# Kernel optimization log

Hardware: AMD Instinct MI355X
Metric: run time of the kernel (lower is better)

Reference implementation:

```python
import jax, jax.numpy as jnp
import numpy as np

B, H, I = 64, 4096, 14336   # batch, hidden, expert intermediate
NLUT = 4096                 # 2**L_bits, L=12
W_SCALE = 0.02              # payload['W_scale'] (same for all three here)


def _rademacher(key, shape):
    return jnp.where(jax.random.bernoulli(key, 0.5, shape), 1.0, -1.0).astype(jnp.float32)


def setup_inputs() -> dict:
    key = jax.random.key(0)
    ks = jax.random.split(key, 14)
    inp = {
        "x": jax.random.normal(ks[0], (B, H), jnp.float32),
        "lut_gate": jax.random.normal(ks[1], (NLUT,), jnp.float32) * 0.05,
        "lut_up": jax.random.normal(ks[2], (NLUT,), jnp.float32) * 0.05,
        "lut_down": jax.random.normal(ks[3], (NLUT,), jnp.float32) * 0.05,
        "gate_walks": jax.random.randint(ks[4], (I, H), 0, NLUT, jnp.int32),
        "up_walks": jax.random.randint(ks[5], (I, H), 0, NLUT, jnp.int32),
        "down_walks": jax.random.randint(ks[6], (H, I), 0, NLUT, jnp.int32),
        "gate_sign_l": _rademacher(ks[7], (I,)),
        "gate_sign_r": _rademacher(ks[8], (H,)),
        "up_sign_l": _rademacher(ks[9], (I,)),
        "up_sign_r": _rademacher(ks[10], (H,)),
        "down_sign_l": _rademacher(ks[11], (H,)),
        "down_sign_r": _rademacher(ks[12], (I,)),
    }
    return inp


def _dequant(lut, walks, sign_l, sign_r):
    # trellis-walk LUT gather per weight element, then row/col signs and scalar scale
    # walks: (out, in) int codes; lut: (NLUT,)
    return (lut[walks] * sign_l[:, None] * sign_r[None, :]) * W_SCALE


def reference(x, lut_gate, lut_up, lut_down,
              gate_walks, up_walks, down_walks,
              gate_sign_l, gate_sign_r, up_sign_l, up_sign_r,
              down_sign_l, down_sign_r):
    W_gate = _dequant(lut_gate, gate_walks, gate_sign_l, gate_sign_r)  # (I, H)
    W_up = _dequant(lut_up, up_walks, up_sign_l, up_sign_r)            # (I, H)
    W_down = _dequant(lut_down, down_walks, down_sign_l, down_sign_r)  # (H, I)
    gate_out = jax.nn.silu(x @ W_gate.T)   # (B, I)
    up_out = x @ W_up.T                    # (B, I)
    hidden = gate_out * up_out
    return hidden @ W_down.T               # (B, H)
```

## Files before the change

### kernel.cpp

```cpp
#include <hip/hip_runtime.h>
#include <hip/hip_bf16.h>

#define HD   4096
#define ID   14336
#define NB   64
#define NLUTN 4096
#define DKS  8

typedef __attribute__((ext_vector_type(8))) short short8;
typedef __attribute__((ext_vector_type(4))) float f32x4;

__device__ __forceinline__ unsigned short f2bf(float f) {
  __hip_bfloat16 h = __float2bfloat16(f);
  return __builtin_bit_cast(unsigned short, h);
}

__device__ __forceinline__ void gll16(const int* g, void* l) {
  __builtin_amdgcn_global_load_lds(
      (const __attribute__((address_space(1))) int*)g,
      (__attribute__((address_space(3))) int*)l, 16, 0, 0);
}

__global__ __launch_bounds__(256) void prep_kernel(
    const float* __restrict__ x, const float* __restrict__ gsr,
    const float* __restrict__ usr,
    unsigned short* __restrict__ xgB, unsigned short* __restrict__ xuB)
{
  int u = blockIdx.x * 256 + threadIdx.x;
  int b = u & 63, k8 = u >> 6;
  const float* xp = x + (size_t)b * HD + k8 * 8;
  float4 x0 = ((const float4*)xp)[0];
  float4 x1 = ((const float4*)xp)[1];
  const float* gp = gsr + k8 * 8;
  const float* up = usr + k8 * 8;
  float4 g0 = ((const float4*)gp)[0], g1 = ((const float4*)gp)[1];
  float4 u0 = ((const float4*)up)[0], u1 = ((const float4*)up)[1];
  ushort4 og0 = make_ushort4(f2bf(x0.x*g0.x), f2bf(x0.y*g0.y), f2bf(x0.z*g0.z), f2bf(x0.w*g0.w));
  ushort4 og1 = make_ushort4(f2bf(x1.x*g1.x), f2bf(x1.y*g1.y), f2bf(x1.z*g1.z), f2bf(x1.w*g1.w));
  ushort4 ou0 = make_ushort4(f2bf(x0.x*u0.x), f2bf(x0.y*u0.y), f2bf(x0.z*u0.z), f2bf(x0.w*u0.w));
  ushort4 ou1 = make_ushort4(f2bf(x1.x*u1.x), f2bf(x1.y*u1.y), f2bf(x1.z*u1.z), f2bf(x1.w*u1.w));
  ((ushort4*)(xgB + (size_t)u*8))[0] = og0;
  ((ushort4*)(xgB + (size_t)u*8))[1] = og1;
  ((ushort4*)(xuB + (size_t)u*8))[0] = ou0;
  ((ushort4*)(xuB + (size_t)u*8))[1] = ou1;
}

__global__ __launch_bounds__(128, 2) void gate_up_kernel(
    const int* __restrict__ gw, const int* __restrict__ uw,
    const float* __restrict__ lutg_f, const float* __restrict__ lutu_f,
    const unsigned short* __restrict__ xgB, const unsigned short* __restrict__ xuB,
    const float* __restrict__ gsl, const float* __restrict__ usl,
    const float* __restrict__ dsr,
    unsigned short* __restrict__ hidB)
{
  __shared__ unsigned short lutg[NLUTN];
  __shared__ unsigned short lutu[NLUTN];
  __shared__ __align__(16) int cbuf[2][3][512];
  __shared__ f32x4 red[4][64];

  const int tid  = threadIdx.x;
  const int lane = tid & 63;
  const int w    = tid >> 6;

  for (int i = tid; i < NLUTN/4; i += 128) {
    float4 g = ((const float4*)lutg_f)[i];
    float4 u = ((const float4*)lutu_f)[i];
    ((ushort4*)lutg)[i] = make_ushort4(f2bf(g.x), f2bf(g.y), f2bf(g.z), f2bf(g.w));
    ((ushort4*)lutu)[i] = make_ushort4(f2bf(u.x), f2bf(u.y), f2bf(u.z), f2bf(u.w));
  }
  __syncthreads();

  const unsigned short* lut = w ? lutu : lutg;
  const int* cw = w ? uw : gw;
  const unsigned short* xB = w ? xuB : xgB;

  const int col  = lane & 15;
  const int quad = lane >> 4;
  const int m0   = blockIdx.x * 16;
  const int r8   = lane >> 3;
  const int j    = lane & 7;
  const int jx   = (j ^ r8) << 2;
  const int xsw  = (col & 7) << 4;

  const int* src0 = cw + (size_t)(m0 + r8) * HD + jx;
  const int* src1 = cw + (size_t)(m0 + 8 + r8) * HD + jx;

  int* b0 = &cbuf[w][0][0];
  int* b1 = &cbuf[w][1][0];
  int* b2 = &cbuf[w][2][0];

  const f32x4 z = {0.f, 0.f, 0.f, 0.f};
  f32x4 acc[4] = {z, z, z, z};

  gll16(src0 + 0, b0); gll16(src1 + 0, (char*)b0 + 1024);
  short8 xv[4];
  {
    size_t xo = ((size_t)quad * 64 + col) * 8;
    #pragma unroll
    for (int t = 0; t < 4; ++t)
      xv[t] = __builtin_bit_cast(short8, *(const int4*)(xB + xo + t*128));
  }
  gll16(src0 + 32, b1); gll16(src1 + 32, (char*)b1 + 1024);

  const int NIT = HD / 32;
  for (int it = 0; it < NIT; ++it) {
    asm volatile("s_waitcnt vmcnt(6)" ::: "memory");
    __builtin_amdgcn_sched_barrier(0);

    const char* cg = (const char*)b0;
    int4 ca = *(const int4*)(cg + col*128 + (((quad<<5) + 0 ) ^ xsw));
    int4 cb = *(const int4*)(cg + col*128 + (((quad<<5) + 16) ^ xsw));
    short8 af;
    af[0] = (short)lut[ca.x]; af[1] = (short)lut[ca.y];
    af[2] = (short)lut[ca.z]; af[3] = (short)lut[ca.w];
    af[4] = (short)lut[cb.x]; af[5] = (short)lut[cb.y];
    af[6] = (short)lut[cb.z]; af[7] = (short)lut[cb.w];

    const int kx = (it+1 < NIT) ? (it+1)*32 : 0;
    short8 xn[4];
    {
      size_t xo = ((size_t)((kx >> 3) + quad) * 64 + col) * 8;
      #pragma unroll
      for (int t = 0; t < 4; ++t)
        xn[t] = __builtin_bit_cast(short8, *(const int4*)(xB + xo + t*128));
    }

    const int ks = (it+2 < NIT) ? (it+2)*32 : 0;
    gll16(src0 + ks, b2); gll16(src1 + ks, (char*)b2 + 1024);

    #pragma unroll
    for (int t = 0; t < 4; ++t)
      acc[t] = __builtin_amdgcn_mfma_f32_16x16x32_bf16(af, xv[t], acc[t], 0, 0, 0);

    #pragma unroll
    for (int t = 0; t < 4; ++t) xv[t] = xn[t];
    int* tmp = b0; b0 = b1; b1 = b2; b2 = tmp;
  }

  if (w == 1) {
    #pragma unroll
    for (int t = 0; t < 4; ++t) red[t][lane] = acc[t];
  }
  __syncthreads();
  if (w == 0) {
    const int mrow = m0 + quad * 4;
    float sg[4], su[4], sd[4];
    #pragma unroll
    for (int r = 0; r < 4; ++r) {
      sg[r] = 0.02f * gsl[mrow + r];
      su[r] = 0.02f * usl[mrow + r];
      sd[r] = dsr[mrow + r];
    }
    #pragma unroll
    for (int t = 0; t < 4; ++t) {
      f32x4 au = red[t][lane];
      int b = t*16 + col;
      float g0 = acc[t][0]*sg[0], u0 = au[0]*su[0];
      float g1 = acc[t][1]*sg[1], u1 = au[1]*su[1];
      float g2 = acc[t][2]*sg[2], u2 = au[2]*su[2];
      float g3 = acc[t][3]*sg[3], u3 = au[3]*su[3];
      ushort4 hv;
      hv.x = f2bf((g0 / (1.f + __expf(-g0))) * u0 * sd[0]);
      hv.y = f2bf((g1 / (1.f + __expf(-g1))) * u1 * sd[1]);
      hv.z = f2bf((g2 / (1.f + __expf(-g2))) * u2 * sd[2]);
      hv.w = f2bf((g3 / (1.f + __expf(-g3))) * u3 * sd[3]);
      *(ushort4*)(hidB + ((size_t)((mrow >> 3)*64 + b))*8 + (quad & 1)*4) = hv;
    }
  }
}

__global__ __launch_bounds__(128, 2) void down_kernel(
    const int* __restrict__ dw, const float* __restrict__ lutd_f,
    const unsigned short* __restrict__ hidB,
    const float* __restrict__ dsl,
    float* __restrict__ out)
{
  __shared__ unsigned short lutd[NLUTN];
  __shared__ __align__(16) int cbuf[2][3][512];

  const int tid  = threadIdx.x;
  const int lane = tid & 63;
  const int w    = tid >> 6;

  for (int i = tid; i < NLUTN/4; i += 128) {
    float4 d = ((const float4*)lutd_f)[i];
    ((ushort4*)lutd)[i] = make_ushort4(f2bf(d.x), f2bf(d.y), f2bf(d.z), f2bf(d.w));
  }
  __syncthreads();

  const int col  = lane & 15;
  const int quad = lane >> 4;
  const int m0   = blockIdx.x * 32 + w * 16;
  const int r8   = lane >> 3;
  const int j    = lane & 7;
  const int jx   = (j ^ r8) << 2;
  const int xsw  = (col & 7) << 4;

  const int kbeg = blockIdx.y * (ID / DKS);
  const int NIT  = (ID / DKS) / 32;

  const int* src0 = dw + (size_t)(m0 + r8) * ID + kbeg + jx;
  const int* src1 = dw + (size_t)(m0 + 8 + r8) * ID + kbeg + jx;

  int* b0 = &cbuf[w][0][0];
  int* b1 = &cbuf[w][1][0];
  int* b2 = &cbuf[w][2][0];

  const f32x4 z = {0.f, 0.f, 0.f, 0.f};
  f32x4 acc[4] = {z, z, z, z};

  gll16(src0 + 0, b0); gll16(src1 + 0, (char*)b0 + 1024);
  short8 xv[4];
  {
    size_t xo = ((size_t)((kbeg >> 3) + quad) * 64 + col) * 8;
    #pragma unroll
    for (int t = 0; t < 4; ++t)
      xv[t] = __builtin_bit_cast(short8, *(const int4*)(hidB + xo + t*128));
  }
  gll16(src0 + 32, b1); gll16(src1 + 32, (char*)b1 + 1024);

  for (int it = 0; it < NIT; ++it) {
    asm volatile("s_waitcnt vmcnt(6)" ::: "memory");
    __builtin_amdgcn_sched_barrier(0);

    const char* cd = (const char*)b0;
    int4 ca = *(const int4*)(cd + col*128 + (((quad<<5) + 0 ) ^ xsw));
    int4 cb = *(const int4*)(cd + col*128 + (((quad<<5) + 16) ^ xsw));
    short8 af;
    af[0] = (short)lutd[ca.x]; af[1] = (short)lutd[ca.y];
    af[2] = (short)lutd[ca.z]; af[3] = (short)lutd[ca.w];
    af[4] = (short)lutd[cb.x]; af[5] = (short)lutd[cb.y];
    af[6] = (short)lutd[cb.z]; af[7] = (short)lutd[cb.w];

    const int kx = (it+1 < NIT) ? kbeg + (it+1)*32 : kbeg;
    short8 xn[4];
    {
      size_t xo = ((size_t)((kx >> 3) + quad) * 64 + col) * 8;
      #pragma unroll
      for (int t = 0; t < 4; ++t)
        xn[t] = __builtin_bit_cast(short8, *(const int4*)(hidB + xo + t*128));
    }

    const int ks = (it+2 < NIT) ? (it+2)*32 : 0;
    gll16(src0 + ks, b2); gll16(src1 + ks, (char*)b2 + 1024);

    #pragma unroll
    for (int t = 0; t < 4; ++t)
      acc[t] = __builtin_amdgcn_mfma_f32_16x16x32_bf16(af, xv[t], acc[t], 0, 0, 0);

    #pragma unroll
    for (int t = 0; t < 4; ++t) xv[t] = xn[t];
    int* tmp = b0; b0 = b1; b1 = b2; b2 = tmp;
  }

  const int mrow = m0 + quad * 4;
  float sc[4];
  #pragma unroll
  for (int r = 0; r < 4; ++r) sc[r] = 0.02f * dsl[mrow + r];
  #pragma unroll
  for (int t = 0; t < 4; ++t) {
    int b = t*16 + col;
    #pragma unroll
    for (int r = 0; r < 4; ++r)
      atomicAdd(&out[(size_t)b * HD + mrow + r], acc[t][r] * sc[r]);
  }
}

extern "C" void kernel_launch(void* const* d_in, const int* in_sizes, int n_in,
                              void* d_out, int out_size, void* d_ws, size_t ws_size,
                              hipStream_t stream) {
  const float* x    = (const float*)d_in[0];
  const float* lutg = (const float*)d_in[1];
  const float* lutu = (const float*)d_in[2];
  const float* lutd = (const float*)d_in[3];
  const int*   gw   = (const int*)d_in[4];
  const int*   uw   = (const int*)d_in[5];
  const int*   dw   = (const int*)d_in[6];
  const float* gsl  = (const float*)d_in[7];
  const float* gsr  = (const float*)d_in[8];
  const float* usl  = (const float*)d_in[9];
  const float* usr  = (const float*)d_in[10];
  const float* dsl  = (const float*)d_in[11];
  const float* dsr  = (const float*)d_in[12];
  float* out = (float*)d_out;

  unsigned short* xgB  = (unsigned short*)d_ws;
  unsigned short* xuB  = xgB + (size_t)NB * HD;
  unsigned short* hidB = xuB + (size_t)NB * HD;

  hipMemsetAsync(d_out, 0, (size_t)NB * HD * sizeof(float), stream);
  prep_kernel<<<(NB*HD/8 + 255)/256, 256, 0, stream>>>(x, gsr, usr, xgB, xuB);
  gate_up_kernel<<<ID/16, 128, 0, stream>>>(gw, uw, lutg, lutu, xgB, xuB,
                                            gsl, usl, dsr, hidB);
  down_kernel<<<dim3(HD/32, DKS), 128, 0, stream>>>(dw, lutd, hidB, dsl, out);
}
```

Baseline: 675.2 us.

## Enlarge gate/up and down tiles, stage activations through LDS with async loads

The gate/up kernel now runs 256-thread blocks covering 64 output rows. Each wave computes two 16-row MFMA tiles. Activations are loaded into LDS with global_load_lds in a 4-deep ring instead of per-wave register loads, and a block barrier is added each iteration. The down kernel likewise uses 256-thread blocks of 64 rows with shared LDS-staged hidden activations, and swaps the MFMA operand order so that atomic adds write contiguous h columns. The goal is to cut redundant activation reads and make code fetches more coalesced and better pipelined. The cost is extra per-iteration barriers and lower occupancy for gate/up (launch bounds of 1 block).

```diff
diff --git a/kernel.cpp b/kernel.cpp
--- a/kernel.cpp
+++ b/kernel.cpp
@@ -45,7 +45,7 @@
   ((ushort4*)(xuB + (size_t)u*8))[1] = ou1;
 }
 
-__global__ __launch_bounds__(128, 2) void gate_up_kernel(
+__global__ __launch_bounds__(256, 1) void gate_up_kernel(
     const int* __restrict__ gw, const int* __restrict__ uw,
     const float* __restrict__ lutg_f, const float* __restrict__ lutu_f,
     const unsigned short* __restrict__ xgB, const unsigned short* __restrict__ xuB,
@@ -55,14 +55,15 @@
 {
   __shared__ unsigned short lutg[NLUTN];
   __shared__ unsigned short lutu[NLUTN];
-  __shared__ __align__(16) int cbuf[2][3][512];
-  __shared__ f32x4 red[4][64];
+  __shared__ __align__(16) char arena[4*4*4096 + 4*2*4096];
 
   const int tid  = threadIdx.x;
   const int lane = tid & 63;
   const int w    = tid >> 6;
-
-  for (int i = tid; i < NLUTN/4; i += 128) {
+  const int m    = w >> 1;
+  const int r    = w & 1;
+
+  for (int i = tid; i < NLUTN/4; i += 256) {
     float4 g = ((const float4*)lutg_f)[i];
     float4 u = ((const float4*)lutu_f)[i];
     ((ushort4*)lutg)[i] = make_ushort4(f2bf(g.x), f2bf(g.y), f2bf(g.z), f2bf(g.w));
@@ -70,119 +71,133 @@
   }
   __syncthreads();
 
-  const unsigned short* lut = w ? lutu : lutg;
-  const int* cw = w ? uw : gw;
-  const unsigned short* xB = w ? xuB : xgB;
+  const unsigned short* lut = m ? lutu : lutg;
+  const int* cw = m ? uw : gw;
+  const unsigned short* xB = m ? xuB : xgB;
 
   const int col  = lane & 15;
   const int quad = lane >> 4;
-  const int m0   = blockIdx.x * 16;
+  const int m0   = blockIdx.x * 64;
   const int r8   = lane >> 3;
   const int j    = lane & 7;
   const int jx   = (j ^ r8) << 2;
   const int xsw  = (col & 7) << 4;
 
-  const int* src0 = cw + (size_t)(m0 + r8) * HD + jx;
-  const int* src1 = cw + (size_t)(m0 + 8 + r8) * HD + jx;
-
-  int* b0 = &cbuf[w][0][0];
-  int* b1 = &cbuf[w][1][0];
-  int* b2 = &cbuf[w][2][0];
+  const int* csrc[4];
+  #pragma unroll
+  for (int g = 0; g < 4; ++g)
+    csrc[g] = cw + (size_t)(m0 + r*32 + g*8 + r8) * HD + jx;
+  const int* xsrc = (const int*)xB + lane * 4;
 
   const f32x4 z = {0.f, 0.f, 0.f, 0.f};
-  f32x4 acc[4] = {z, z, z, z};
-
-  gll16(src0 + 0, b0); gll16(src1 + 0, (char*)b0 + 1024);
-  short8 xv[4];
-  {
-    size_t xo = ((size_t)quad * 64 + col) * 8;
+  f32x4 acc[2][4] = {{z,z,z,z},{z,z,z,z}};
+
+  const int NIT = HD / 32;
+
+  #define GU_STAGE(IT, RR) {                                          \
+    int ko_ = ((IT) < NIT) ? (IT)*32 : 0;                             \
+    int xc_ = ((IT) < NIT) ? (IT)     : 0;                            \
+    char* cb_ = arena + ((RR)*4 + w) * 4096;                          \
+    gll16(csrc[0] + ko_, cb_);                                        \
+    gll16(csrc[1] + ko_, cb_ + 1024);                                 \
+    gll16(csrc[2] + ko_, cb_ + 2048);                                 \
+    gll16(csrc[3] + ko_, cb_ + 3072);                                 \
+    char* xb_ = arena + 65536 + ((RR)*2 + m) * 4096 + r*2048;         \
+    gll16(xsrc + xc_*1024 + (r*2  )*256, xb_);                        \
+    gll16(xsrc + xc_*1024 + (r*2+1)*256, xb_ + 1024);                 \
+  }
+
+  GU_STAGE(0, 0);
+  GU_STAGE(1, 1);
+
+  for (int it = 0; it < NIT; ++it) {
+    GU_STAGE(it + 2, (it + 2) & 3);
+    asm volatile("s_waitcnt vmcnt(12)" ::: "memory");
+    __builtin_amdgcn_s_barrier();
+    __builtin_amdgcn_sched_barrier(0);
+
+    const char* cb = arena + ((it & 3)*4 + w) * 4096;
+    const char* xb = arena + 65536 + ((it & 3)*2 + m) * 4096;
+
+    short8 af[2];
+    #pragma unroll
+    for (int s = 0; s < 2; ++s) {
+      int4 ca = *(const int4*)(cb + s*2048 + col*128 + (((quad<<5)     ) ^ xsw));
+      int4 cc = *(const int4*)(cb + s*2048 + col*128 + (((quad<<5) + 16) ^ xsw));
+      af[s][0] = (short)lut[ca.x]; af[s][1] = (short)lut[ca.y];
+      af[s][2] = (short)lut[ca.z]; af[s][3] = (short)lut[ca.w];
+      af[s][4] = (short)lut[cc.x]; af[s][5] = (short)lut[cc.y];
+      af[s][6] = (short)lut[cc.z]; af[s][7] = (short)lut[cc.w];
+    }
+    short8 xv[4];
     #pragma unroll
     for (int t = 0; t < 4; ++t)
-      xv[t] = __builtin_bit_cast(short8, *(const int4*)(xB + xo + t*128));
-  }
-  gll16(src0 + 32, b1); gll16(src1 + 32, (char*)b1 + 1024);
-
-  const int NIT = HD / 32;
-  for (int it = 0; it < NIT; ++it) {
-    asm volatile("s_waitcnt vmcnt(6)" ::: "memory");
-    __builtin_amdgcn_sched_barrier(0);
-
-    const char* cg = (const char*)b0;
-    int4 ca = *(const int4*)(cg + col*128 + (((quad<<5) + 0 ) ^ xsw));
-    int4 cb = *(const int4*)(cg + col*128 + (((quad<<5) + 16) ^ xsw));
-    short8 af;
-    af[0] = (short)lut[ca.x]; af[1] = (short)lut[ca.y];
-    af[2] = (short)lut[ca.z]; af[3] = (short)lut[ca.w];
-    af[4] = (short)lut[cb.x]; af[5] = (short)lut[cb.y];
-    af[6] = (short)lut[cb.z]; af[7] = (short)lut[cb.w];
-
-    const int kx = (it+1 < NIT) ? (it+1)*32 : 0;
-    short8 xn[4];
-    {
-      size_t xo = ((size_t)((kx >> 3) + quad) * 64 + col) * 8;
+      xv[t] = __builtin_bit_cast(short8,
+                *(const int4*)(xb + quad*1024 + t*256 + col*16));
+
+    #pragma unroll
+    for (int t = 0; t < 4; ++t)
+      #pragma unroll
+      for (int s = 0; s < 2; ++s)
+        acc[s][t] = __builtin_amdgcn_mfma_f32_16x16x32_bf16(af[s], xv[t], acc[s][t], 0, 0, 0);
+  }
+  #undef GU_STAGE
+
+  asm volatile("s_waitcnt vmcnt(0)" ::: "memory");
+  __syncthreads();
+
+  if (w >= 2) {
+    #pragma unroll
+    for (int s = 0; s < 2; ++s)
       #pragma unroll
       for (int t = 0; t < 4; ++t)
-        xn[t] = __builtin_bit_cast(short8, *(const int4*)(xB + xo + t*128));
+        *(f32x4*)(arena + ((((w-2)*2 + s)*4 + t)*64 + lane)*16) = acc[s][t];
+  }
+  __syncthreads();
+  if (w < 2) {
+    #pragma unroll
+    for (int s = 0; s < 2; ++s) {
+      const int mrow = m0 + w*32 + s*16 + quad*4;
+      float sg[4], su[4], sd[4];
+      #pragma unroll
+      for (int rr = 0; rr < 4; ++rr) {
+        sg[rr] = 0.02f * gsl[mrow + rr];
+        su[rr] = 0.02f * usl[mrow + rr];
+        sd[rr] = dsr[mrow + rr];
+      }
+      #pragma unroll
+      for (int t = 0; t < 4; ++t) {
+        f32x4 au = *(const f32x4*)(arena + (((w*2 + s)*4 + t)*64 + lane)*16);
+        int b = t*16 + col;
+        float g0 = acc[s][t][0]*sg[0], u0 = au[0]*su[0];
+        float g1 = acc[s][t][1]*sg[1], u1 = au[1]*su[1];
+        float g2 = acc[s][t][2]*sg[2], u2 = au[2]*su[2];
+        float g3 = acc[s][t][3]*sg[3], u3 = au[3]*su[3];
+        ushort4 hv;
+        hv.x = f2bf((g0 / (1.f + __expf(-g0))) * u0 * sd[0]);
+        hv.y = f2bf((g1 / (1.f + __expf(-g1))) * u1 * sd[1]);
+        hv.z = f2bf((g2 / (1.f + __expf(-g2))) * u2 * sd[2]);
+        hv.w = f2bf((g3 / (1.f + __expf(-g3))) * u3 * sd[3]);
+        *(ushort4*)(hidB + ((size_t)((mrow >> 3)*64 + b))*8 + (quad & 1)*4) = hv;
+      }
     }
-
-    const int ks = (it+2 < NIT) ? (it+2)*32 : 0;
-    gll16(src0 + ks, b2); gll16(src1 + ks, (char*)b2 + 1024);
-
-    #pragma unroll
-    for (int t = 0; t < 4; ++t)
-      acc[t] = __builtin_amdgcn_mfma_f32_16x16x32_bf16(af, xv[t], acc[t], 0, 0, 0);
-
-    #pragma unroll
-    for (int t = 0; t < 4; ++t) xv[t] = xn[t];
-    int* tmp = b0; b0 = b1; b1 = b2; b2 = tmp;
-  }
-
-  if (w == 1) {
-    #pragma unroll
-    for (int t = 0; t < 4; ++t) red[t][lane] = acc[t];
-  }
-  __syncthreads();
-  if (w == 0) {
-    const int mrow = m0 + quad * 4;
-    float sg[4], su[4], sd[4];
-    #pragma unroll
-    for (int r = 0; r < 4; ++r) {
-      sg[r] = 0.02f * gsl[mrow + r];
-      su[r] = 0.02f * usl[mrow + r];
-      sd[r] = dsr[mrow + r];
-    }
-    #pragma unroll
-    for (int t = 0; t < 4; ++t) {
-      f32x4 au = red[t][lane];
-      int b = t*16 + col;
-      float g0 = acc[t][0]*sg[0], u0 = au[0]*su[0];
-      float g1 = acc[t][1]*sg[1], u1 = au[1]*su[1];
-      float g2 = acc[t][2]*sg[2], u2 = au[2]*su[2];
-      float g3 = acc[t][3]*sg[3], u3 = au[3]*su[3];
-      ushort4 hv;
-      hv.x = f2bf((g0 / (1.f + __expf(-g0))) * u0 * sd[0]);
-      hv.y = f2bf((g1 / (1.f + __expf(-g1))) * u1 * sd[1]);
-      hv.z = f2bf((g2 / (1.f + __expf(-g2))) * u2 * sd[2]);
-      hv.w = f2bf((g3 / (1.f + __expf(-g3))) * u3 * sd[3]);
-      *(ushort4*)(hidB + ((size_t)((mrow >> 3)*64 + b))*8 + (quad & 1)*4) = hv;
-    }
-  }
-}
-
-__global__ __launch_bounds__(128, 2) void down_kernel(
+  }
+}
+
+__global__ __launch_bounds__(256, 2) void down_kernel(
     const int* __restrict__ dw, const float* __restrict__ lutd_f,
     const unsigned short* __restrict__ hidB,
     const float* __restrict__ dsl,
     float* __restrict__ out)
 {
   __shared__ unsigned short lutd[NLUTN];
-  __shared__ __align__(16) int cbuf[2][3][512];
+  __shared__ __align__(16) char arena[4*4*2048 + 4*4096];
 
   const int tid  = threadIdx.x;
   const int lane = tid & 63;
   const int w    = tid >> 6;
 
-  for (int i = tid; i < NLUTN/4; i += 128) {
+  for (int i = tid; i < NLUTN/4; i += 256) {
     float4 d = ((const float4*)lutd_f)[i];
     ((ushort4*)lutd)[i] = make_ushort4(f2bf(d.x), f2bf(d.y), f2bf(d.z), f2bf(d.w));
   }
@@ -190,7 +205,7 @@
 
   const int col  = lane & 15;
   const int quad = lane >> 4;
-  const int m0   = blockIdx.x * 32 + w * 16;
+  const int m0   = blockIdx.x * 64;
   const int r8   = lane >> 3;
   const int j    = lane & 7;
   const int jx   = (j ^ r8) << 2;
@@ -199,70 +214,63 @@
   const int kbeg = blockIdx.y * (ID / DKS);
   const int NIT  = (ID / DKS) / 32;
 
-  const int* src0 = dw + (size_t)(m0 + r8) * ID + kbeg + jx;
-  const int* src1 = dw + (size_t)(m0 + 8 + r8) * ID + kbeg + jx;
-
-  int* b0 = &cbuf[w][0][0];
-  int* b1 = &cbuf[w][1][0];
-  int* b2 = &cbuf[w][2][0];
+  const int* csrc0 = dw + (size_t)(m0 + w*16     + r8) * ID + kbeg + jx;
+  const int* csrc1 = dw + (size_t)(m0 + w*16 + 8 + r8) * ID + kbeg + jx;
+  const int* xsrc  = (const int*)hidB + kbeg*32 + lane*4;
 
   const f32x4 z = {0.f, 0.f, 0.f, 0.f};
   f32x4 acc[4] = {z, z, z, z};
 
-  gll16(src0 + 0, b0); gll16(src1 + 0, (char*)b0 + 1024);
-  short8 xv[4];
-  {
-    size_t xo = ((size_t)((kbeg >> 3) + quad) * 64 + col) * 8;
-    #pragma unroll
-    for (int t = 0; t < 4; ++t)
-      xv[t] = __builtin_bit_cast(short8, *(const int4*)(hidB + xo + t*128));
-  }
-  gll16(src0 + 32, b1); gll16(src1 + 32, (char*)b1 + 1024);
+  #define DN_STAGE(IT, RR) {                                          \
+    int ko_ = ((IT) < NIT) ? (IT)*32 : 0;                             \
+    int xc_ = ((IT) < NIT) ? (IT)     : 0;                            \
+    char* cb_ = arena + ((RR)*4 + w) * 2048;                          \
+    gll16(csrc0 + ko_, cb_);                                          \
+    gll16(csrc1 + ko_, cb_ + 1024);                                   \
+    gll16(xsrc + xc_*1024 + w*256, arena + 32768 + (RR)*4096 + w*1024); \
+  }
+
+  DN_STAGE(0, 0);
+  DN_STAGE(1, 1);
 
   for (int it = 0; it < NIT; ++it) {
+    DN_STAGE(it + 2, (it + 2) & 3);
     asm volatile("s_waitcnt vmcnt(6)" ::: "memory");
+    __builtin_amdgcn_s_barrier();
     __builtin_amdgcn_sched_barrier(0);
 
-    const char* cd = (const char*)b0;
-    int4 ca = *(const int4*)(cd + col*128 + (((quad<<5) + 0 ) ^ xsw));
-    int4 cb = *(const int4*)(cd + col*128 + (((quad<<5) + 16) ^ xsw));
+    const char* cb = arena + ((it & 3)*4 + w) * 2048;
+    const char* xb = arena + 32768 + (it & 3) * 4096;
+
+    int4 ca = *(const int4*)(cb + col*128 + (((quad<<5)     ) ^ xsw));
+    int4 cc = *(const int4*)(cb + col*128 + (((quad<<5) + 16) ^ xsw));
     short8 af;
     af[0] = (short)lutd[ca.x]; af[1] = (short)lutd[ca.y];
     af[2] = (short)lutd[ca.z]; af[3] = (short)lutd[ca.w];
-    af[4] = (short)lutd[cb.x]; af[5] = (short)lutd[cb.y];
-    af[6] = (short)lutd[cb.z]; af[7] = (short)lutd[cb.w];
-
-    const int kx = (it+1 < NIT) ? kbeg + (it+1)*32 : kbeg;
-    short8 xn[4];
-    {
-      size_t xo = ((size_t)((kx >> 3) + quad) * 64 + col) * 8;
-      #pragma unroll
-      for (int t = 0; t < 4; ++t)
-        xn[t] = __builtin_bit_cast(short8, *(const int4*)(hidB + xo + t*128));
-    }
-
-    const int ks = (it+2 < NIT) ? (it+2)*32 : 0;
-    gll16(src0 + ks, b2); gll16(src1 + ks, (char*)b2 + 1024);
-
+    af[4] = (short)lutd[cc.x]; af[5] = (short)lutd[cc.y];
+    af[6] = (short)lutd[cc.z]; af[7] = (short)lutd[cc.w];
+
+    short8 xv[4];
     #pragma unroll
     for (int t = 0; t < 4; ++t)
-      acc[t] = __builtin_amdgcn_mfma_f32_16x16x32_bf16(af, xv[t], acc[t], 0, 0, 0);
-
-    #pragma unroll
-    for (int t = 0; t < 4; ++t) xv[t] = xn[t];
-    int* tmp = b0; b0 = b1; b1 = b2; b2 = tmp;
-  }
-
-  const int mrow = m0 + quad * 4;
-  float sc[4];
-  #pragma unroll
-  for (int r = 0; r < 4; ++r) sc[r] = 0.02f * dsl[mrow + r];
+      xv[t] = __builtin_bit_cast(short8,
+                *(const int4*)(xb + quad*1024 + t*256 + col*16));
+
+    #pragma unroll
+    for (int t = 0; t < 4; ++t)
+      acc[t] = __builtin_amdgcn_mfma_f32_16x16x32_bf16(xv[t], af, acc[t], 0, 0, 0);
+  }
+  #undef DN_STAGE
+
+  const int h = m0 + w*16 + col;
+  const float sd = 0.02f * dsl[h];
   #pragma unroll
   for (int t = 0; t < 4; ++t) {
-    int b = t*16 + col;
-    #pragma unroll
-    for (int r = 0; r < 4; ++r)
-      atomicAdd(&out[(size_t)b * HD + mrow + r], acc[t][r] * sc[r]);
+    #pragma unroll
+    for (int rr = 0; rr < 4; ++rr) {
+      int b = t*16 + quad*4 + rr;
+      atomicAdd(&out[(size_t)b * HD + h], acc[t][rr] * sd);
+    }
   }
 }
 
@@ -290,7 +298,7 @@
 
   hipMemsetAsync(d_out, 0, (size_t)NB * HD * sizeof(float), stream);
   prep_kernel<<<(NB*HD/8 + 255)/256, 256, 0, stream>>>(x, gsr, usr, xgB, xuB);
-  gate_up_kernel<<<ID/16, 128, 0, stream>>>(gw, uw, lutg, lutu, xgB, xuB,
+  gate_up_kernel<<<ID/64, 256, 0, stream>>>(gw, uw, lutg, lutu, xgB, xuB,
                                             gsl, usl, dsr, hidB);
-  down_kernel<<<dim3(HD/32, DKS), 128, 0, stream>>>(dw, lutd, hidB, dsl, out);
-}
+  down_kernel<<<dim3(HD/64, DKS), 256, 0, stream>>>(dw, lutd, hidB, dsl, out);
+}
```

Result: faster. 651.3 us (-3.5%).

## Split K across waves in gate/up, double down split-K, transpose down MFMA for coalesced atomics

Applied to the files above, without the earlier changes.

The gate/up kernel now uses four waves per block: each of the gate and up products is split into two K halves, and the halves are reduced through shared memory that reuses the code buffer. The down kernel's split-K factor rises from 8 to 16, and its MFMA operands are swapped so that each lane's output column is contiguous in hidden. That makes the atomicAdds to the output coalesced across lanes. The aim is more parallelism to hide the latency of the gather-heavy LUT dequant and cheaper atomics, at the cost of extra shared-memory reductions, more atomic traffic, and higher register and LDS pressure.

```diff
diff --git a/kernel.cpp b/kernel.cpp
--- a/kernel.cpp
+++ b/kernel.cpp
@@ -5,7 +5,7 @@
 #define ID   14336
 #define NB   64
 #define NLUTN 4096
-#define DKS  8
+#define DKS  16
 
 typedef __attribute__((ext_vector_type(8))) short short8;
 typedef __attribute__((ext_vector_type(4))) float f32x4;
@@ -45,7 +45,7 @@
   ((ushort4*)(xuB + (size_t)u*8))[1] = ou1;
 }
 
-__global__ __launch_bounds__(128, 2) void gate_up_kernel(
+__global__ __launch_bounds__(256, 4) void gate_up_kernel(
     const int* __restrict__ gw, const int* __restrict__ uw,
     const float* __restrict__ lutg_f, const float* __restrict__ lutu_f,
     const unsigned short* __restrict__ xgB, const unsigned short* __restrict__ xuB,
@@ -55,14 +55,15 @@
 {
   __shared__ unsigned short lutg[NLUTN];
   __shared__ unsigned short lutu[NLUTN];
-  __shared__ __align__(16) int cbuf[2][3][512];
-  __shared__ f32x4 red[4][64];
+  __shared__ __align__(16) int cbuf[4][3][512];
 
   const int tid  = threadIdx.x;
   const int lane = tid & 63;
   const int w    = tid >> 6;
-
-  for (int i = tid; i < NLUTN/4; i += 128) {
+  const int m    = w & 1;
+  const int kh   = w >> 1;
+
+  for (int i = tid; i < NLUTN/4; i += 256) {
     float4 g = ((const float4*)lutg_f)[i];
     float4 u = ((const float4*)lutu_f)[i];
     ((ushort4*)lutg)[i] = make_ushort4(f2bf(g.x), f2bf(g.y), f2bf(g.z), f2bf(g.w));
@@ -70,9 +71,9 @@
   }
   __syncthreads();
 
-  const unsigned short* lut = w ? lutu : lutg;
-  const int* cw = w ? uw : gw;
-  const unsigned short* xB = w ? xuB : xgB;
+  const unsigned short* lut = m ? lutu : lutg;
+  const int* cw = m ? uw : gw;
+  const unsigned short* xB = m ? xuB : xgB;
 
   const int col  = lane & 15;
   const int quad = lane >> 4;
@@ -82,8 +83,11 @@
   const int jx   = (j ^ r8) << 2;
   const int xsw  = (col & 7) << 4;
 
-  const int* src0 = cw + (size_t)(m0 + r8) * HD + jx;
-  const int* src1 = cw + (size_t)(m0 + 8 + r8) * HD + jx;
+  const int kbeg = kh * (HD/2);
+  const int NIT  = (HD/2) / 32;
+
+  const int* src0 = cw + (size_t)(m0 + r8) * HD + kbeg + jx;
+  const int* src1 = cw + (size_t)(m0 + 8 + r8) * HD + kbeg + jx;
 
   int* b0 = &cbuf[w][0][0];
   int* b1 = &cbuf[w][1][0];
@@ -95,14 +99,13 @@
   gll16(src0 + 0, b0); gll16(src1 + 0, (char*)b0 + 1024);
   short8 xv[4];
   {
-    size_t xo = ((size_t)quad * 64 + col) * 8;
+    size_t xo = ((size_t)((kbeg >> 3) + quad) * 64 + col) * 8;
     #pragma unroll
     for (int t = 0; t < 4; ++t)
       xv[t] = __builtin_bit_cast(short8, *(const int4*)(xB + xo + t*128));
   }
   gll16(src0 + 32, b1); gll16(src1 + 32, (char*)b1 + 1024);
 
-  const int NIT = HD / 32;
   for (int it = 0; it < NIT; ++it) {
     asm volatile("s_waitcnt vmcnt(6)" ::: "memory");
     __builtin_amdgcn_sched_barrier(0);
@@ -116,7 +119,7 @@
     af[4] = (short)lut[cb.x]; af[5] = (short)lut[cb.y];
     af[6] = (short)lut[cb.z]; af[7] = (short)lut[cb.w];
 
-    const int kx = (it+1 < NIT) ? (it+1)*32 : 0;
+    const int kx = (it+1 < NIT) ? kbeg + (it+1)*32 : kbeg;
     short8 xn[4];
     {
       size_t xo = ((size_t)((kx >> 3) + quad) * 64 + col) * 8;
@@ -137,9 +140,23 @@
     int* tmp = b0; b0 = b1; b1 = b2; b2 = tmp;
   }
 
-  if (w == 1) {
-    #pragma unroll
-    for (int t = 0; t < 4; ++t) red[t][lane] = acc[t];
+  asm volatile("s_waitcnt vmcnt(0)" ::: "memory");
+  __syncthreads();
+  f32x4* red = (f32x4*)&cbuf[0][0][0];
+
+  if (kh == 1) {
+    #pragma unroll
+    for (int t = 0; t < 4; ++t) red[(m*4 + t)*64 + lane] = acc[t];
+  }
+  __syncthreads();
+  if (kh == 0) {
+    #pragma unroll
+    for (int t = 0; t < 4; ++t) acc[t] += red[(m*4 + t)*64 + lane];
+  }
+  __syncthreads();
+  if (kh == 0 && m == 1) {
+    #pragma unroll
+    for (int t = 0; t < 4; ++t) red[t*64 + lane] = acc[t];
   }
   __syncthreads();
   if (w == 0) {
@@ -153,7 +170,7 @@
     }
     #pragma unroll
     for (int t = 0; t < 4; ++t) {
-      f32x4 au = red[t][lane];
+      f32x4 au = red[t*64 + lane];
       int b = t*16 + col;
       float g0 = acc[t][0]*sg[0], u0 = au[0]*su[0];
       float g1 = acc[t][1]*sg[1], u1 = au[1]*su[1];
@@ -169,7 +186,7 @@
   }
 }
 
-__global__ __launch_bounds__(128, 2) void down_kernel(
+__global__ __launch_bounds__(128, 4) void down_kernel(
     const int* __restrict__ dw, const float* __restrict__ lutd_f,
     const unsigned short* __restrict__ hidB,
     const float* __restrict__ dsl,
@@ -246,23 +263,22 @@
 
     #pragma unroll
     for (int t = 0; t < 4; ++t)
-      acc[t] = __builtin_amdgcn_mfma_f32_16x16x32_bf16(af, xv[t], acc[t], 0, 0, 0);
+      acc[t] = __builtin_amdgcn_mfma_f32_16x16x32_bf16(xv[t], af, acc[t], 0, 0, 0);
 
     #pragma unroll
     for (int t = 0; t < 4; ++t) xv[t] = xn[t];
     int* tmp = b0; b0 = b1; b1 = b2; b2 = tmp;
   }
 
-  const int mrow = m0 + quad * 4;
-  float sc[4];
-  #pragma unroll
-  for (int r = 0; r < 4; ++r) sc[r] = 0.02f * dsl[mrow + r];
+  const int h = m0 + col;
+  const float sd = 0.02f * dsl[h];
   #pragma unroll
   for (int t = 0; t < 4; ++t) {
-    int b = t*16 + col;
-    #pragma unroll
-    for (int r = 0; r < 4; ++r)
-      atomicAdd(&out[(size_t)b * HD + mrow + r], acc[t][r] * sc[r]);
+    #pragma unroll
+    for (int rr = 0; rr < 4; ++rr) {
+      int b = t*16 + quad*4 + rr;
+      atomicAdd(&out[(size_t)b * HD + h], acc[t][rr] * sd);
+    }
   }
 }
 
@@ -290,7 +306,7 @@
 
   hipMemsetAsync(d_out, 0, (size_t)NB * HD * sizeof(float), stream);
   prep_kernel<<<(NB*HD/8 + 255)/256, 256, 0, stream>>>(x, gsr, usr, xgB, xuB);
-  gate_up_kernel<<<ID/16, 128, 0, stream>>>(gw, uw, lutg, lutu, xgB, xuB,
+  gate_up_kernel<<<ID/16, 256, 0, stream>>>(gw, uw, lutg, lutu, xgB, xuB,
                                             gsl, usl, dsr, hidB);
   down_kernel<<<dim3(HD/32, DKS), 128, 0, stream>>>(dw, lutd, hidB, dsl, out);
 }
```

Measured after the change: 657.5 us. -2.6%, faster.
